# Performance work log

Measured on AMD Instinct MI355X. Metric: run time of the kernel, lower is better.

The kernel has to match this reference:

```python
import jax, jax.numpy as jnp
import numpy as np

B, N = 256, 128  # batch, n_neurons; n_equations = 4*N


def _pos(k, shape):
    # positive parameters (conductances, capacitance, time constants)
    return jax.random.uniform(k, shape, jnp.float32, 0.5, 1.5)


def setup_inputs() -> dict:
    key = jax.random.key(0)
    ks = jax.random.split(key, 17)
    return {
        "y": jax.random.normal(ks[0], (B, 4 * N), jnp.float32),
        "Ic": jax.random.normal(ks[1], (B,), jnp.float32),  # I(t) evaluated, per-batch current
        "C": _pos(ks[2], (N,)),
        "g_Na": _pos(ks[3], (N,)),
        "E_Na": jax.random.normal(ks[4], (N,), jnp.float32),
        "g_K": _pos(ks[5], (N,)),
        "E_K": jax.random.normal(ks[6], (N,), jnp.float32),
        "g_L": _pos(ks[7], (N,)),
        "E_L": jax.random.normal(ks[8], (N,), jnp.float32),
        "m_inf": jax.random.uniform(ks[9], (N,), jnp.float32),
        "tau_m": _pos(ks[10], (N,)),
        "h_inf": jax.random.uniform(ks[11], (N,), jnp.float32),
        "tau_h": _pos(ks[12], (N,)),
        "n_inf": jax.random.uniform(ks[13], (N,), jnp.float32),
        "tau_n": _pos(ks[14], (N,)),
        "g_C": 0.1 * _pos(ks[15], (N, N)),
    }


def _diag_embed(x):
    # x: (..., N) -> (..., N, N) with x on the diagonal
    return x[..., :, None] * jnp.eye(x.shape[-1], dtype=x.dtype)


def reference(y, Ic, C, g_Na, E_Na, g_K, E_K, g_L, E_L,
              m_inf, tau_m, h_inf, tau_h, n_inf, tau_n, g_C):
    V = y[..., 0::4]  # (B, N)
    m = y[..., 1::4]
    h = y[..., 2::4]
    n = y[..., 3::4]

    invC = 1.0 / C  # (N,)
    Vdot = invC * (-g_Na * m ** 3 * h * (V - E_Na)
                   - g_K * n ** 4 * (V - E_K)
                   - g_L * (V - E_L)
                   + Ic[..., None])
    # coupling: sum_j g_C[i,j] * (V_i - V_j) / C[j]  (C broadcasts over last axis, as in torch)
    dV = jnp.sum(g_C[None, :, :] * (V[..., :, None] - V[..., None, :]) * invC[None, None, :], axis=-1)
    Vdot = Vdot + dV
    mdot = (m_inf - m) / tau_m
    hdot = (h_inf - h) / tau_h
    ndot = (n_inf - n) / tau_n
    # interleave back to (B, 4N) matching y[..., 0::4] layout
    ydot = jnp.stack([Vdot, mdot, hdot, ndot], axis=-1).reshape(y.shape)

    E = y.shape[-1]
    J = jnp.zeros(y.shape + (E,), dtype=y.dtype)

    gC_over_C = g_C * invC[None, :]  # (N, N), column-wise division as in torch broadcast
    JVV = (_diag_embed(invC * (-g_L - g_Na * h * m ** 3 - g_K * n ** 4))
           - gC_over_C[None, :, :]
           + jnp.eye(N, dtype=y.dtype) * jnp.sum(gC_over_C))
    J = J.at[..., 0::4, 0::4].set(JVV)
    J = J.at[..., 0::4, 1::4].set(_diag_embed(-invC * (3.0 * g_Na * h * m ** 2 * (V - E_Na))))
    J = J.at[..., 0::4, 2::4].set(_diag_embed(-invC * (g_Na * m ** 3 * (V - E_Na))))
    J = J.at[..., 0::4, 3::4].set(_diag_embed(-invC * (4.0 * g_K * n ** 3 * (V - E_K))))
    J = J.at[..., 1::4, 1::4].set(jnp.diag(-1.0 / tau_m))
    J = J.at[..., 2::4, 2::4].set(jnp.diag(-1.0 / tau_h))
    J = J.at[..., 3::4, 3::4].set(jnp.diag(-1.0 / tau_n))

    return ydot, J
```

## Files before the change

kernel.cpp:

```cpp
#include <hip/hip_runtime.h>

#define BATCH 256
#define NN    128
#define EDIM  512

typedef float vf4 __attribute__((ext_vector_type(4)));

__global__ __launch_bounds__(512) void hh_k1(
    const float* __restrict__ y,     const float* __restrict__ Ic,
    const float* __restrict__ C,     const float* __restrict__ g_Na,
    const float* __restrict__ E_Na,  const float* __restrict__ g_K,
    const float* __restrict__ E_K,   const float* __restrict__ g_L,
    const float* __restrict__ E_L,   const float* __restrict__ m_inf,
    const float* __restrict__ tau_m, const float* __restrict__ h_inf,
    const float* __restrict__ tau_h, const float* __restrict__ n_inf,
    const float* __restrict__ tau_n, const float* __restrict__ g_C,
    float* __restrict__ ydot_out,    float4* __restrict__ jtab,
    float* __restrict__ invC_out,    float* __restrict__ nitab)
{
    __shared__ float sInvC[NN];
    __shared__ float sW[NN];
    __shared__ float sRed[NN];
    __shared__ float sS;

    const int b  = blockIdx.x;
    const int t  = threadIdx.x;
    const int i  = t >> 2;
    const int jq = t & 3;

    if (t < NN) {
        const float ic = 1.0f / C[t];
        sInvC[t] = ic;
        sW[t] = y[(size_t)b * EDIM + 4 * t] * ic;
    }
    __syncthreads();

    float rowS = 0.f, dotW = 0.f;
    const float4* grow = (const float4*)(g_C + (i << 7) + (jq << 5));
#pragma unroll
    for (int j4 = 0; j4 < 8; ++j4) {
        const float4 g = grow[j4];
        const int j = (jq << 5) + j4 * 4;
        rowS += g.x * sInvC[j] + g.y * sInvC[j + 1] + g.z * sInvC[j + 2] + g.w * sInvC[j + 3];
        dotW += g.x * sW[j]    + g.y * sW[j + 1]    + g.z * sW[j + 2]    + g.w * sW[j + 3];
    }
    rowS += __shfl_xor(rowS, 1);  rowS += __shfl_xor(rowS, 2);
    dotW += __shfl_xor(dotW, 1);  dotW += __shfl_xor(dotW, 2);

    if (jq == 0) sRed[i] = rowS;
    __syncthreads();
    if (t < 64) {
        float v = sRed[t] + sRed[t + 64];
        v += __shfl_xor(v, 1);  v += __shfl_xor(v, 2);  v += __shfl_xor(v, 4);
        v += __shfl_xor(v, 8);  v += __shfl_xor(v, 16); v += __shfl_xor(v, 32);
        if (t == 0) sS = v;
    }
    __syncthreads();

    if (jq == 0) {
        const float S = sS;
        const float4 yv = ((const float4*)(y + (size_t)b * EDIM))[i];
        const float V = yv.x, m = yv.y, h = yv.z, n = yv.w;
        const float invC = sInvC[i];
        const float dV = V * rowS - dotW;

        const float m2 = m * m, m3 = m2 * m;
        const float n2 = n * n, n3 = n2 * n, n4 = n3 * n;
        const float gna = g_Na[i], ena = E_Na[i];
        const float gk  = g_K[i],  ek  = E_K[i];
        const float gl  = g_L[i],  el  = E_L[i];

        const float Vdot = invC * (-gna * m3 * h * (V - ena)
                                   - gk * n4 * (V - ek)
                                   - gl * (V - el)
                                   + Ic[b]) + dV;
        const float itm = 1.0f / tau_m[i];
        const float ith = 1.0f / tau_h[i];
        const float itn = 1.0f / tau_n[i];

        ((float4*)(ydot_out + (size_t)b * EDIM))[i] =
            make_float4(Vdot, (m_inf[i] - m) * itm, (h_inf[i] - h) * ith,
                        (n_inf[i] - n) * itn);

        const float jvv = invC * (-gl - gna * h * m3 - gk * n4) + S;
        const float jvm = -invC * (3.0f * gna * h * m2 * (V - ena));
        const float jvh = -invC * (gna * m3 * (V - ena));
        const float jvn = -invC * (4.0f * gk * n3 * (V - ek));
        jtab[(b << 7) + i] = make_float4(jvv, jvm, jvh, jvn);

        if (b == 0) {
            invC_out[i]       = invC;
            nitab[i]          = -itm;
            nitab[NN + i]     = -ith;
            nitab[2 * NN + i] = -itn;
        }
    }
}

__global__ __launch_bounds__(256) void hh_k2(
    const float4* __restrict__ jtab, const float* __restrict__ invC,
    const float* __restrict__ nitab, const float* __restrict__ g_C,
    vf4* __restrict__ J)
{
    const int t = threadIdx.x;
    const int q = t & 31;
    const unsigned g = blockIdx.x * 8u + (t >> 5);
    const int a = g >> 15;
    const unsigned s = g & 32767u;
    const int b = s >> 7;
    const int i = s & 127;
    const unsigned row = ((unsigned)b << 9) | ((unsigned)i << 2) | (unsigned)a;

    vf4* __restrict__ Jrow = J + (size_t)row * 128;

    if (a == 0) {
        const float4 jv = jtab[(b << 7) + i];
#pragma unroll
        for (int k = 0; k < 4; ++k) {
            const int j = q + 32 * k;
            float v0 = -g_C[(i << 7) + j] * invC[j];
            float v1 = 0.f, v2 = 0.f, v3 = 0.f;
            if (j == i) { v0 += jv.x; v1 = jv.y; v2 = jv.z; v3 = jv.w; }
            const vf4 v = {v0, v1, v2, v3};
            Jrow[j] = v;
        }
    } else {
        const float nit = nitab[((a - 1) << 7) + i];
#pragma unroll
        for (int k = 0; k < 4; ++k) {
            const int j = q + 32 * k;
            vf4 v = {0.f, 0.f, 0.f, 0.f};
            if (j == i) {
                if (a == 1)      v.y = nit;
                else if (a == 2) v.z = nit;
                else             v.w = nit;
            }
            Jrow[j] = v;
        }
    }
}

extern "C" void kernel_launch(void* const* d_in, const int* in_sizes, int n_in,
                              void* d_out, int out_size, void* d_ws, size_t ws_size,
                              hipStream_t stream) {
    const float* y     = (const float*)d_in[0];
    const float* Ic    = (const float*)d_in[1];
    const float* C     = (const float*)d_in[2];
    const float* g_Na  = (const float*)d_in[3];
    const float* E_Na  = (const float*)d_in[4];
    const float* g_K   = (const float*)d_in[5];
    const float* E_K   = (const float*)d_in[6];
    const float* g_L   = (const float*)d_in[7];
    const float* E_L   = (const float*)d_in[8];
    const float* m_inf = (const float*)d_in[9];
    const float* tau_m = (const float*)d_in[10];
    const float* h_inf = (const float*)d_in[11];
    const float* tau_h = (const float*)d_in[12];
    const float* n_inf = (const float*)d_in[13];
    const float* tau_n = (const float*)d_in[14];
    const float* g_C   = (const float*)d_in[15];

    float* ydot = (float*)d_out;
    vf4*   J    = (vf4*)((float*)d_out + (size_t)BATCH * EDIM);

    float4* jtab = (float4*)d_ws;
    float*  invC = (float*)((char*)d_ws + (size_t)BATCH * NN * sizeof(float4));
    float*  nit  = invC + NN;

    hh_k1<<<BATCH, 512, 0, stream>>>(y, Ic, C, g_Na, E_Na, g_K, E_K, g_L, E_L,
                                     m_inf, tau_m, h_inf, tau_h, n_inf, tau_n,
                                     g_C, ydot, jtab, invC, nit);

    hh_k2<<<131072 / 8, 256, 0, stream>>>(jtab, invC, nit, g_C, J);
}
```

Before: 288.0 us.

## Fuse Jacobian fill into per-batch kernel, dropping second launch and workspace

Merges the two kernels into one per-batch block that computes the diagonal Jacobian terms into shared memory and then writes the full 512x512 Jacobian slice directly. Each thread handles one column and one of four row classes, looping over 128 rows. This removes the intermediate workspace table and a second launch, but it cuts the grid to 256 blocks. That may limit memory-level parallelism for the very large store-bound output.

```diff
diff --git a/kernel.cpp b/kernel.cpp
--- a/kernel.cpp
+++ b/kernel.cpp
@@ -6,7 +6,7 @@
 
 typedef float vf4 __attribute__((ext_vector_type(4)));
 
-__global__ __launch_bounds__(512) void hh_k1(
+__global__ __launch_bounds__(512) void hh_fused(
     const float* __restrict__ y,     const float* __restrict__ Ic,
     const float* __restrict__ C,     const float* __restrict__ g_Na,
     const float* __restrict__ E_Na,  const float* __restrict__ g_K,
@@ -15,13 +15,14 @@
     const float* __restrict__ tau_m, const float* __restrict__ h_inf,
     const float* __restrict__ tau_h, const float* __restrict__ n_inf,
     const float* __restrict__ tau_n, const float* __restrict__ g_C,
-    float* __restrict__ ydot_out,    float4* __restrict__ jtab,
-    float* __restrict__ invC_out,    float* __restrict__ nitab)
+    float* __restrict__ ydot_out,    vf4* __restrict__ J)
 {
-    __shared__ float sInvC[NN];
-    __shared__ float sW[NN];
-    __shared__ float sRed[NN];
-    __shared__ float sS;
+    __shared__ float  sInvC[NN];
+    __shared__ float  sW[NN];
+    __shared__ float  sRed[NN];
+    __shared__ float  sS;
+    __shared__ float4 sJV[NN];
+    __shared__ float  sNit[3 * NN];
 
     const int b  = blockIdx.x;
     const int t  = threadIdx.x;
@@ -32,6 +33,10 @@
         const float ic = 1.0f / C[t];
         sInvC[t] = ic;
         sW[t] = y[(size_t)b * EDIM + 4 * t] * ic;
+    } else {
+        const int k = t - NN;
+        const float* tau = (k < NN) ? tau_m : (k < 2 * NN ? tau_h : tau_n);
+        sNit[k] = -1.0f / tau[k & (NN - 1)];
     }
     __syncthreads();
 
@@ -74,9 +79,9 @@
                                    - gk * n4 * (V - ek)
                                    - gl * (V - el)
                                    + Ic[b]) + dV;
-        const float itm = 1.0f / tau_m[i];
-        const float ith = 1.0f / tau_h[i];
-        const float itn = 1.0f / tau_n[i];
+        const float itm = -sNit[i];
+        const float ith = -sNit[NN + i];
+        const float itn = -sNit[2 * NN + i];
 
         ((float4*)(ydot_out + (size_t)b * EDIM))[i] =
             make_float4(Vdot, (m_inf[i] - m) * itm, (h_inf[i] - h) * ith,
@@ -86,56 +91,36 @@
         const float jvm = -invC * (3.0f * gna * h * m2 * (V - ena));
         const float jvh = -invC * (gna * m3 * (V - ena));
         const float jvn = -invC * (4.0f * gk * n3 * (V - ek));
-        jtab[(b << 7) + i] = make_float4(jvv, jvm, jvh, jvn);
+        sJV[i] = make_float4(jvv, jvm, jvh, jvn);
+    }
+    __syncthreads();
 
-        if (b == 0) {
-            invC_out[i]       = invC;
-            nitab[i]          = -itm;
-            nitab[NN + i]     = -ith;
-            nitab[2 * NN + i] = -itn;
-        }
-    }
-}
-
-__global__ __launch_bounds__(256) void hh_k2(
-    const float4* __restrict__ jtab, const float* __restrict__ invC,
-    const float* __restrict__ nitab, const float* __restrict__ g_C,
-    vf4* __restrict__ J)
-{
-    const int t = threadIdx.x;
-    const int q = t & 31;
-    const unsigned g = blockIdx.x * 8u + (t >> 5);
-    const int a = g >> 15;
-    const unsigned s = g & 32767u;
-    const int b = s >> 7;
-    const int i = s & 127;
-    const unsigned row = ((unsigned)b << 9) | ((unsigned)i << 2) | (unsigned)a;
-
-    vf4* __restrict__ Jrow = J + (size_t)row * 128;
+    const int a = t >> 7;
+    const int q = t & 127;
+    vf4* __restrict__ Jp = J + ((size_t)b * EDIM + a) * (EDIM / 4) + q;
 
     if (a == 0) {
-        const float4 jv = jtab[(b << 7) + i];
-#pragma unroll
-        for (int k = 0; k < 4; ++k) {
-            const int j = q + 32 * k;
-            float v0 = -g_C[(i << 7) + j] * invC[j];
-            float v1 = 0.f, v2 = 0.f, v3 = 0.f;
-            if (j == i) { v0 += jv.x; v1 = jv.y; v2 = jv.z; v3 = jv.w; }
-            const vf4 v = {v0, v1, v2, v3};
-            Jrow[j] = v;
+        const float  icq = sInvC[q];
+        const float4 jvq = sJV[q];
+        const float* __restrict__ gq = g_C + q;
+#pragma unroll 4
+        for (int r = 0; r < NN; ++r) {
+            const float gv = gq[r << 7];
+            vf4 v;
+            v.x = -gv * icq;
+            v.y = 0.f; v.z = 0.f; v.w = 0.f;
+            if (r == q) { v.x += jvq.x; v.y = jvq.y; v.z = jvq.z; v.w = jvq.w; }
+            Jp[(size_t)r * EDIM] = v;
         }
     } else {
-        const float nit = nitab[((a - 1) << 7) + i];
-#pragma unroll
-        for (int k = 0; k < 4; ++k) {
-            const int j = q + 32 * k;
+        const float d = sNit[((a - 1) << 7) + q];
+        vf4 dv = {0.f, 0.f, 0.f, 0.f};
+        if (a == 1) dv.y = d; else if (a == 2) dv.z = d; else dv.w = d;
+#pragma unroll 4
+        for (int r = 0; r < NN; ++r) {
             vf4 v = {0.f, 0.f, 0.f, 0.f};
-            if (j == i) {
-                if (a == 1)      v.y = nit;
-                else if (a == 2) v.z = nit;
-                else             v.w = nit;
-            }
-            Jrow[j] = v;
+            if (r == q) v = dv;
+            Jp[(size_t)r * EDIM] = v;
         }
     }
 }
@@ -163,13 +148,7 @@
     float* ydot = (float*)d_out;
     vf4*   J    = (vf4*)((float*)d_out + (size_t)BATCH * EDIM);
 
-    float4* jtab = (float4*)d_ws;
-    float*  invC = (float*)((char*)d_ws + (size_t)BATCH * NN * sizeof(float4));
-    float*  nit  = invC + NN;
-
-    hh_k1<<<BATCH, 512, 0, stream>>>(y, Ic, C, g_Na, E_Na, g_K, E_K, g_L, E_L,
-                                     m_inf, tau_m, h_inf, tau_h, n_inf, tau_n,
-                                     g_C, ydot, jtab, invC, nit);
-
-    hh_k2<<<131072 / 8, 256, 0, stream>>>(jtab, invC, nit, g_C, J);
+    hh_fused<<<BATCH, 512, 0, stream>>>(y, Ic, C, g_Na, E_Na, g_K, E_K, g_L, E_L,
+                                        m_inf, tau_m, h_inf, tau_h, n_inf, tau_n,
+                                        g_C, ydot, J);
 }
```

After: 289.3 us. No clear change (+0.5%).
